# Performance work log

Hardware: AMD Instinct MI355X
Metric: run time of the kernel (lower is better)

The kernel has to match this reference:

```python
import jax, jax.numpy as jnp
import numpy as np

B, NZ, L = 8, 16, 512
E, DM, NH, HD = 256, 512, 16, 32
FF, NL, E1D, PDIM, PMAX = 1024, 8, 32, 64, 24
EPS_LN = 1e-5
EPS_D = 1e-12


def _ln(x, g, b):
    m = jnp.mean(x, axis=-1, keepdims=True)
    v = jnp.mean((x - m) ** 2, axis=-1, keepdims=True)
    return (x - m) / jnp.sqrt(v + EPS_LN) * g + b


def setup_inputs() -> dict:
    key = jax.random.key(0)
    ks = iter(jax.random.split(key, 32))
    rn = lambda shape, fan: jax.random.normal(next(ks), shape, jnp.float32) / np.float32(np.sqrt(fan))
    inp = {
        "z": jax.random.normal(next(ks), (B, NZ, L), jnp.float32),
        "x": jax.random.uniform(next(ks), (B, 20, L), jnp.float32),
        # embeddings
        "pos_table": rn((2 * PMAX + 1, PDIM), 1.0),
        "aa_table": rn((20, E1D), 1.0),
        # embed_x: Linear(nz,E), relu, Linear(E,E)
        "ex_w1": rn((NZ, E), NZ), "ex_b1": jnp.zeros((E,), jnp.float32),
        "ex_w2": rn((E, E), E), "ex_b2": jnp.zeros((E,), jnp.float32),
        # per-layer stacked params
        "Wq": rn((NL, E, DM), E), "Wk": rn((NL, E, DM), E), "Wv": rn((NL, E, DM), E),
        "Wo": rn((NL, DM, E), DM), "bo": jnp.zeros((NL, E), jnp.float32),
        "W2d": rn((NL, PDIM, NH), PDIM), "b2d": jnp.zeros((NL, NH), jnp.float32),
        "W1": rn((NL, E + E1D, FF), E + E1D), "b1": jnp.zeros((NL, FF), jnp.float32),
        "W2": rn((NL, FF, E), FF), "b2": jnp.zeros((NL, E), jnp.float32),
        "g1": jnp.ones((NL, E), jnp.float32), "be1": jnp.zeros((NL, E), jnp.float32),
        "g2": jnp.ones((NL, E), jnp.float32), "be2": jnp.zeros((NL, E), jnp.float32),
        # mlp_3d: Linear(E,E), relu, Linear(E,3)
        "m3_w1": rn((E, E), E), "m3_b1": jnp.zeros((E,), jnp.float32),
        "m3_w2": rn((E, 3), E), "m3_b2": jnp.zeros((3,), jnp.float32),
    }
    return inp


def reference(z, x, pos_table, aa_table, ex_w1, ex_b1, ex_w2, ex_b2,
              Wq, Wk, Wv, Wo, bo, W2d, b2d, W1, b1, W2, b2,
              g1, be1, g2, be2, m3_w1, m3_b1, m3_w2, m3_b2):
    Bn, _, Ln = z.shape
    h = jnp.transpose(z, (0, 2, 1))  # (B, L, nz)
    # relative-position bins: argmin over integer bins == clip to [-PMAX, PMAX]
    rel = jnp.arange(Ln)[None, :] - jnp.arange(Ln)[:, None]
    bins = jnp.clip(rel, -PMAX, PMAX) + PMAX
    pe = pos_table[bins]  # (L, L, PDIM), batch-replicated
    e_aa = aa_table[jnp.argmax(x, axis=1)]  # (B, L, E1D)
    # embed_x MLP
    h = jax.nn.relu(h @ ex_w1 + ex_b1) @ ex_w2 + ex_b2  # (B, L, E)
    scale = np.float32(1.0 / np.sqrt(DM))  # dp_attn_norm='d_model'
    for i in range(NL):
        q = (h @ Wq[i]).reshape(Bn, Ln, NH, HD) * scale
        k = (h @ Wk[i]).reshape(Bn, Ln, NH, HD)
        v = (h @ Wv[i]).reshape(Bn, Ln, NH, HD)
        # learned pairwise bias: mlp_2d then transpose(1,3).transpose(2,3) -> bias[h,i,j] = out[i,j,h]
        bias = jnp.einsum('lmp,ph->hlm', pe, W2d[i]) + b2d[i][:, None, None]
        scores = jnp.einsum('blhd,bmhd->bhlm', q, k) + bias[None]
        attn = jax.nn.softmax(scores, axis=-1)
        o = jnp.einsum('bhlm,bmhd->blhd', attn, v).reshape(Bn, Ln, DM)
        h = _ln(h + (o @ Wo[i] + bo[i]), g1[i], be1[i])
        um = jnp.concatenate([h, e_aa], axis=-1)  # (B, L, E+E1D)
        s2 = jax.nn.relu(um @ W1[i] + b1[i]) @ W2[i] + b2[i]
        h = _ln(h + s2, g2[i], be2[i])
    r = jax.nn.relu(h @ m3_w1 + m3_b1) @ m3_w2 + m3_b2  # (B, L, 3)
    # distance map (get_coords=False path)
    d = jnp.sqrt(jnp.sum((r[:, None, :, :] - r[:, :, None, :]) ** 2, axis=-1) + EPS_D)
    return d  # (B, L, L)
```

## Files before the change

kernel.cpp:

```cpp
#include <hip/hip_runtime.h>
#include <math.h>

constexpr int Bn = 8, NZ = 16, Ln = 512;
constexpr int E = 256, DM = 512, NH = 16, HD = 32;
constexpr int FF = 1024, NL = 8, E1D = 32, PDIM = 64, PMAX = 24;
constexpr int ROWS = Bn * Ln;
constexpr float QSCALE = 0.04419417382415922f;

typedef __attribute__((ext_vector_type(8))) short bf16x8;
typedef __attribute__((ext_vector_type(4))) float floatx4;

__device__ inline unsigned short f2b(float f) {
  union { float f; unsigned u; } v; v.f = f;
  unsigned r = (v.u + 0x7FFF + ((v.u >> 16) & 1)) >> 16;
  return (unsigned short)r;
}
__device__ inline float b2f(unsigned short u) {
  union { unsigned u; float f; } v; v.u = ((unsigned)u) << 16; return v.f;
}

__global__ __launch_bounds__(256) void transpose_qkv(
    const float* __restrict__ Wq, const float* __restrict__ Wk,
    const float* __restrict__ Wv, unsigned short* __restrict__ qkvT)
{
  __shared__ float t[32][33];
  int zb = blockIdx.z;
  int which = zb / NL, l = zb % NL;
  const float* s = (which == 0 ? Wq : which == 1 ? Wk : Wv) + (size_t)l * E * DM;
  unsigned short* d = qkvT + (size_t)l * 3 * DM * E + (size_t)which * DM * E;
  int c0 = blockIdx.x * 32, r0 = blockIdx.y * 32;
  int tx = threadIdx.x & 31, ty = threadIdx.x >> 5;
  #pragma unroll
  for (int i = 0; i < 4; ++i)
    t[ty + i * 8][tx] = s[(size_t)(r0 + ty + i * 8) * DM + c0 + tx];
  __syncthreads();
  #pragma unroll
  for (int i = 0; i < 4; ++i)
    d[(size_t)(c0 + ty + i * 8) * E + r0 + tx] = f2b(t[tx][ty + i * 8]);
}

__global__ __launch_bounds__(256) void transpose_bf16(
    const float* __restrict__ src, unsigned short* __restrict__ dst,
    int R, int C, size_t sls, size_t dls)
{
  __shared__ float t[32][33];
  int l = blockIdx.z;
  int c0 = blockIdx.x * 32, r0 = blockIdx.y * 32;
  int tx = threadIdx.x & 31, ty = threadIdx.x >> 5;
  const float* s = src + (size_t)l * sls;
  unsigned short* d = dst + (size_t)l * dls;
  #pragma unroll
  for (int i = 0; i < 4; ++i)
    t[ty + i * 8][tx] = s[(size_t)(r0 + ty + i * 8) * C + c0 + tx];
  __syncthreads();
  #pragma unroll
  for (int i = 0; i < 4; ++i)
    d[(size_t)(c0 + ty + i * 8) * R + r0 + tx] = f2b(t[tx][ty + i * 8]);
}

__global__ __launch_bounds__(256) void embed1_kernel(
    const float* __restrict__ z, const float* __restrict__ x,
    const float* __restrict__ aa,
    const float* __restrict__ w1, const float* __restrict__ b1,
    float* __restrict__ t0, unsigned short* __restrict__ umb)
{
  int row = blockIdx.x;
  int b = row >> 9, l = row & (Ln - 1);
  int t = threadIdx.x;
  __shared__ float zs[NZ];
  __shared__ int am_s;
  if (t < NZ) zs[t] = z[((size_t)b * NZ + t) * Ln + l];
  if (t == 0) {
    const float* xp = x + (size_t)b * 20 * Ln + l;
    int am = 0; float bv = xp[0];
    for (int c = 1; c < 20; ++c) { float vv = xp[(size_t)c * Ln]; if (vv > bv) { bv = vv; am = c; } }
    am_s = am;
  }
  __syncthreads();
  float a1 = b1[t];
  #pragma unroll
  for (int nz = 0; nz < NZ; ++nz) a1 += zs[nz] * w1[nz * E + t];
  t0[(size_t)row * E + t] = fmaxf(a1, 0.f);
  if (t < E1D) umb[(size_t)row * (E + E1D) + E + t] = f2b(aa[am_s * E1D + t]);
}

__global__ __launch_bounds__(256) void bias_kernel(
    const float* __restrict__ pos, const float* __restrict__ W2d,
    const float* __restrict__ b2d, float* __restrict__ bias49)
{
  int layer = blockIdx.x;
  for (int idx = threadIdx.x; idx < NH * 49; idx += 256) {
    int hh = idx / 49, bin = idx % 49;
    float acc = b2d[layer * NH + hh];
    for (int p = 0; p < PDIM; ++p)
      acc += pos[bin * PDIM + p] * W2d[((size_t)layer * PDIM + p) * NH + hh];
    bias49[(size_t)layer * NH * 49 + hh * 49 + bin] = acc;
  }
}

template<int BM, int BN, bool BIAS, bool RELU, bool OUTBF16, bool QKV>
__global__ __launch_bounds__(256) void gemm_mfma(
    const unsigned short* __restrict__ A, const unsigned short* __restrict__ Bt,
    const float* __restrict__ bias,
    float* __restrict__ Cf, unsigned short* __restrict__ Cb, int N, int K)
{
  constexpr int MT = BM / 32, NT = BN / 32;
  __shared__ __align__(16) unsigned short As[BM][40];
  __shared__ __align__(16) unsigned short Bs[BN][40];
  const int tid = threadIdx.x;
  const int wave = tid >> 6, ln = tid & 63;
  const int quad = ln >> 4, l16 = ln & 15;
  const int wm = wave >> 1, wn = wave & 1;
  const int m0 = blockIdx.y * BM, n0 = blockIdx.x * BN;

  floatx4 acc[MT][NT] = {};

  for (int kb = 0; kb < K; kb += 32) {
    __syncthreads();
    #pragma unroll
    for (int it = 0; it < BM / 64; ++it) {
      int c = tid + it * 256;
      int row = c >> 2, cc = (c & 3) * 8;
      *(float4*)&As[row][cc] = *(const float4*)(A + (size_t)(m0 + row) * K + kb + cc);
    }
    #pragma unroll
    for (int it = 0; it < BN / 64; ++it) {
      int c = tid + it * 256;
      int row = c >> 2, cc = (c & 3) * 8;
      *(float4*)&Bs[row][cc] = *(const float4*)(Bt + (size_t)(n0 + row) * K + kb + cc);
    }
    __syncthreads();
    bf16x8 af[MT], bfr[NT];
    #pragma unroll
    for (int i = 0; i < MT; ++i)
      af[i] = *(const bf16x8*)&As[wm * (BM / 2) + i * 16 + l16][quad * 8];
    #pragma unroll
    for (int j = 0; j < NT; ++j)
      bfr[j] = *(const bf16x8*)&Bs[wn * (BN / 2) + j * 16 + l16][quad * 8];
    #pragma unroll
    for (int i = 0; i < MT; ++i)
      #pragma unroll
      for (int j = 0; j < NT; ++j)
        acc[i][j] = __builtin_amdgcn_mfma_f32_16x16x32_bf16(af[i], bfr[j], acc[i][j], 0, 0, 0);
  }

  #pragma unroll
  for (int i = 0; i < MT; ++i)
    #pragma unroll
    for (int j = 0; j < NT; ++j) {
      int col = n0 + wn * (BN / 2) + j * 16 + l16;
      float bv = BIAS ? bias[col] : 0.f;
      float sc = QKV ? (col < 512 ? QSCALE : 1.f) : 1.f;
      #pragma unroll
      for (int r = 0; r < 4; ++r) {
        int rowg = m0 + wm * (BM / 2) + i * 16 + quad * 4 + r;
        float v = acc[i][j][r] * sc + bv;
        if (RELU) v = fmaxf(v, 0.f);
        if (OUTBF16) Cb[(size_t)rowg * N + col] = f2b(v);
        else Cf[(size_t)rowg * N + col] = v;
      }
    }
}

__global__ __launch_bounds__(256) void gemm_n256(
    const unsigned short* __restrict__ A, const unsigned short* __restrict__ Bt,
    const float* __restrict__ bias, const float* __restrict__ resid,
    float* __restrict__ Cf, int K)
{
  __shared__ __align__(16) unsigned short As[32][72];
  __shared__ __align__(16) unsigned short Bs[32][72];
  const int tid = threadIdx.x;
  const int wave = tid >> 6, ln = tid & 63;
  const int quad = ln >> 4, l16 = ln & 15;
  const int wm = wave >> 1, wn = wave & 1;
  const int m0 = blockIdx.y * 32, n0 = blockIdx.x * 32;
  const int srow = tid >> 3, scol = (tid & 7) * 8;

  floatx4 acc = {};

  for (int kb = 0; kb < K; kb += 64) {
    float4 ta = *(const float4*)(A + (size_t)(m0 + srow) * K + kb + scol);
    float4 tb = *(const float4*)(Bt + (size_t)(n0 + srow) * K + kb + scol);
    __syncthreads();
    *(float4*)&As[srow][scol] = ta;
    *(float4*)&Bs[srow][scol] = tb;
    __syncthreads();
    #pragma unroll
    for (int kc = 0; kc < 2; ++kc) {
      bf16x8 af = *(const bf16x8*)&As[wm * 16 + l16][kc * 32 + quad * 8];
      bf16x8 bf = *(const bf16x8*)&Bs[wn * 16 + l16][kc * 32 + quad * 8];
      acc = __builtin_amdgcn_mfma_f32_16x16x32_bf16(af, bf, acc, 0, 0, 0);
    }
  }

  const int col = n0 + wn * 16 + l16;
  const float bv = bias[col];
  #pragma unroll
  for (int r = 0; r < 4; ++r) {
    int rowg = m0 + wm * 16 + quad * 4 + r;
    Cf[(size_t)rowg * 256 + col] = acc[r] + bv + resid[(size_t)rowg * 256 + col];
  }
}

__global__ __launch_bounds__(256) void attn_kernel(
    const unsigned short* __restrict__ qkv, const float* __restrict__ bias49,
    unsigned short* __restrict__ o)
{
  const int i0 = blockIdx.x * 64;
  const int bh = blockIdx.y;
  const int b = bh >> 4, hh = bh & 15;
  const int tid = threadIdx.x;
  const int wave = tid >> 6, ln = tid & 63;
  const int quad = ln >> 4, l16 = ln & 15;

  __shared__ __align__(16) unsigned short Kt[64][40];
  __shared__ __align__(16) unsigned short Vt[32][72];
  __shared__ __align__(16) unsigned short Pw[4][2][16][72];
  __shared__ float bsh[49];

  if (tid < 49) bsh[tid] = bias49[hh * 49 + tid];

  const unsigned short* qkvb = qkv + (size_t)b * Ln * 1536;

  const int qrow = i0 + wave * 16 + l16;
  const bf16x8 qf = *(const bf16x8*)(qkvb + (size_t)qrow * 1536 + hh * 32 + quad * 8);

  float m[4], l[4];
  #pragma unroll
  for (int r = 0; r < 4; ++r) { m[r] = -1e30f; l[r] = 0.f; }
  floatx4 acc_o[2] = {};

  const int krow = tid >> 2, kch = (tid & 3) * 8;
  const int vkey = tid & 63, vch = (tid >> 6) * 8;

  for (int jt = 0; jt < 8; ++jt) {
    const int j0 = jt * 64;
    __syncthreads();
    *(float4*)&Kt[krow][kch] =
        *(const float4*)(qkvb + (size_t)(j0 + krow) * 1536 + 512 + hh * 32 + kch);
    bf16x8 vv = *(const bf16x8*)(qkvb + (size_t)(j0 + vkey) * 1536 + 1024 + hh * 32 + vch);
    #pragma unroll
    for (int i = 0; i < 8; ++i) Vt[vch + i][vkey] = (unsigned short)vv[i];
    __syncthreads();

    floatx4 s4[4];
    #pragma unroll
    for (int t = 0; t < 4; ++t) {
      bf16x8 kf = *(const bf16x8*)&Kt[16 * t + l16][quad * 8];
      s4[t] = __builtin_amdgcn_mfma_f32_16x16x32_bf16(qf, kf, (floatx4){0.f, 0.f, 0.f, 0.f}, 0, 0, 0);
    }
    const int relmin = j0 - (i0 + 63), relmax = j0 + 63 - i0;
    if (relmin >= PMAX) {
      float bc = bsh[48];
      #pragma unroll
      for (int t = 0; t < 4; ++t)
        #pragma unroll
        for (int r = 0; r < 4; ++r) s4[t][r] += bc;
    } else if (relmax <= -PMAX) {
      float bc = bsh[0];
      #pragma unroll
      for (int t = 0; t < 4; ++t)
        #pragma unroll
        for (int r = 0; r < 4; ++r) s4[t][r] += bc;
    } else {
      const int base_rel = (j0 + l16) - (i0 + wave * 16 + quad * 4);
      #pragma unroll
      for (int t = 0; t < 4; ++t)
        #pragma unroll
        for (int r = 0; r < 4; ++r) {
          int rel = base_rel + 16 * t - r;
          rel = rel < -PMAX ? -PMAX : (rel > PMAX ? PMAX : rel);
          s4[t][r] += bsh[rel + PMAX];
        }
    }

    float mloc[4], alpha[4], psum[4];
    #pragma unroll
    for (int r = 0; r < 4; ++r) {
      mloc[r] = fmaxf(fmaxf(s4[0][r], s4[1][r]), fmaxf(s4[2][r], s4[3][r]));
      #pragma unroll
      for (int off = 1; off < 16; off <<= 1)
        mloc[r] = fmaxf(mloc[r], __shfl_xor(mloc[r], off, 64));
      float mnew = fmaxf(m[r], mloc[r]);
      alpha[r] = __expf(m[r] - mnew);
      m[r] = mnew;
      psum[r] = 0.f;
    }
    #pragma unroll
    for (int t = 0; t < 4; ++t)
      #pragma unroll
      for (int r = 0; r < 4; ++r) {
        float p = __expf(s4[t][r] - m[r]);
        s4[t][r] = p;
        psum[r] += p;
      }
    #pragma unroll
    for (int r = 0; r < 4; ++r) {
      #pragma unroll
      for (int off = 1; off < 16; off <<= 1)
        psum[r] += __shfl_xor(psum[r], off, 64);
      l[r] = l[r] * alpha[r] + psum[r];
      acc_o[0][r] *= alpha[r];
      acc_o[1][r] *= alpha[r];
    }

    #pragma unroll
    for (int t = 0; t < 4; ++t)
      #pragma unroll
      for (int r = 0; r < 4; ++r) {
        float p = s4[t][r];
        unsigned short hi = f2b(p);
        unsigned short lo = f2b(p - b2f(hi));
        Pw[wave][0][quad * 4 + r][16 * t + l16] = hi;
        Pw[wave][1][quad * 4 + r][16 * t + l16] = lo;
      }

    #pragma unroll
    for (int kh = 0; kh < 2; ++kh) {
      bf16x8 phi = *(const bf16x8*)&Pw[wave][0][l16][kh * 32 + quad * 8];
      bf16x8 plo = *(const bf16x8*)&Pw[wave][1][l16][kh * 32 + quad * 8];
      #pragma unroll
      for (int nt = 0; nt < 2; ++nt) {
        bf16x8 vf = *(const bf16x8*)&Vt[nt * 16 + l16][kh * 32 + quad * 8];
        acc_o[nt] = __builtin_amdgcn_mfma_f32_16x16x32_bf16(phi, vf, acc_o[nt], 0, 0, 0);
        acc_o[nt] = __builtin_amdgcn_mfma_f32_16x16x32_bf16(plo, vf, acc_o[nt], 0, 0, 0);
      }
    }
  }

  #pragma unroll
  for (int r = 0; r < 4; ++r) {
    float inv = 1.f / l[r];
    size_t rowg = (size_t)b * Ln + i0 + wave * 16 + quad * 4 + r;
    #pragma unroll
    for (int nt = 0; nt < 2; ++nt)
      o[rowg * 512 + hh * 32 + nt * 16 + l16] = f2b(acc_o[nt][r] * inv);
  }
}

__global__ __launch_bounds__(256) void ln_kernel(
    const float* __restrict__ xin, const float* __restrict__ g,
    const float* __restrict__ be, float* __restrict__ hout,
    unsigned short* __restrict__ bout, int bstride)
{
  const int w = threadIdx.x >> 6, lane = threadIdx.x & 63;
  const size_t row = (size_t)blockIdx.x * 4 + w;
  const int c0 = lane * 4;
  float4 v = *(const float4*)(xin + row * E + c0);
  float s = v.x + v.y + v.z + v.w;
  float s2 = v.x * v.x + v.y * v.y + v.z * v.z + v.w * v.w;
  #pragma unroll
  for (int off = 1; off < 64; off <<= 1) {
    s += __shfl_xor(s, off, 64);
    s2 += __shfl_xor(s2, off, 64);
  }
  const float mean = s * (1.f / E);
  const float rstd = rsqrtf(s2 * (1.f / E) - mean * mean + 1e-5f);
  const float4 gv = *(const float4*)(g + c0);
  const float4 bv = *(const float4*)(be + c0);
  float4 y;
  y.x = (v.x - mean) * rstd * gv.x + bv.x;
  y.y = (v.y - mean) * rstd * gv.y + bv.y;
  y.z = (v.z - mean) * rstd * gv.z + bv.z;
  y.w = (v.w - mean) * rstd * gv.w + bv.w;
  *(float4*)(hout + row * E + c0) = y;
  ushort4 yb;
  yb.x = f2b(y.x); yb.y = f2b(y.y); yb.z = f2b(y.z); yb.w = f2b(y.w);
  *(ushort4*)(bout + row * (size_t)bstride + c0) = yb;
}

template<bool RELU, bool BIAS, bool MIRROR>
__global__ __launch_bounds__(256) void gemm64f(
    const float* __restrict__ A, const float* __restrict__ B,
    const float* __restrict__ bias, float* __restrict__ C,
    unsigned short* __restrict__ mir, int N, int K)
{
  __shared__ __align__(16) float As[16][64];
  __shared__ __align__(16) float Bss[16][68];
  const int tid = threadIdx.x;
  const int tx = tid & 15, ty = tid >> 4;
  const int m0 = blockIdx.y * 64, n0 = blockIdx.x * 64;
  const int arow = tid >> 2, acol = (tid & 3) * 4;
  const int brow = tid >> 6, bcol = tid & 63;
  float acc[4][4] = {};
  for (int kb = 0; kb < K; kb += 16) {
    __syncthreads();
    float4 av = *(const float4*)(A + (size_t)(m0 + arow) * K + kb + acol);
    As[acol + 0][arow] = av.x; As[acol + 1][arow] = av.y;
    As[acol + 2][arow] = av.z; As[acol + 3][arow] = av.w;
    #pragma unroll
    for (int kk = 0; kk < 4; ++kk)
      Bss[brow + kk * 4][bcol] = B[(size_t)(kb + brow + kk * 4) * N + n0 + bcol];
    __syncthreads();
    #pragma unroll
    for (int k = 0; k < 16; ++k) {
      float4 a = *(const float4*)&As[k][4 * ty];
      float4 b = *(const float4*)&Bss[k][4 * tx];
      float av4[4] = {a.x, a.y, a.z, a.w};
      float bv4[4] = {b.x, b.y, b.z, b.w};
      #pragma unroll
      for (int ii = 0; ii < 4; ++ii)
        #pragma unroll
        for (int jj = 0; jj < 4; ++jj)
          acc[ii][jj] += av4[ii] * bv4[jj];
    }
  }
  #pragma unroll
  for (int ii = 0; ii < 4; ++ii) {
    size_t row = (size_t)m0 + 4 * ty + ii;
    int col = n0 + 4 * tx;
    float4 vv;
    vv.x = acc[ii][0]; vv.y = acc[ii][1]; vv.z = acc[ii][2]; vv.w = acc[ii][3];
    if (BIAS) {
      float4 bb = *(const float4*)(bias + col);
      vv.x += bb.x; vv.y += bb.y; vv.z += bb.z; vv.w += bb.w;
    }
    if (RELU) {
      vv.x = fmaxf(vv.x, 0.f); vv.y = fmaxf(vv.y, 0.f);
      vv.z = fmaxf(vv.z, 0.f); vv.w = fmaxf(vv.w, 0.f);
    }
    *(float4*)(C + row * N + col) = vv;
    if (MIRROR) {
      ushort4 mv;
      mv.x = f2b(vv.x); mv.y = f2b(vv.y); mv.z = f2b(vv.z); mv.w = f2b(vv.w);
      *(ushort4*)(mir + row * N + col) = mv;
    }
  }
}

__global__ __launch_bounds__(256) void final_r_kernel(
    const float* __restrict__ t1, const float* __restrict__ w2,
    const float* __restrict__ b2, float* __restrict__ r)
{
  int row = blockIdx.x, t = threadIdx.x;
  float xv = t1[(size_t)row * E + t];
  float p0 = xv * w2[t * 3 + 0];
  float p1 = xv * w2[t * 3 + 1];
  float p2 = xv * w2[t * 3 + 2];
  #pragma unroll
  for (int off = 32; off > 0; off >>= 1) {
    p0 += __shfl_down(p0, off, 64);
    p1 += __shfl_down(p1, off, 64);
    p2 += __shfl_down(p2, off, 64);
  }
  __shared__ float red[4][3];
  if ((t & 63) == 0) { int w = t >> 6; red[w][0] = p0; red[w][1] = p1; red[w][2] = p2; }
  __syncthreads();
  if (t < 3)
    r[(size_t)row * 3 + t] = red[0][t] + red[1][t] + red[2][t] + red[3][t] + b2[t];
}

__global__ __launch_bounds__(512) void dist_kernel(
    const float* __restrict__ r, float* __restrict__ out)
{
  int bi = blockIdx.x;
  int j = threadIdx.x;
  int b = bi >> 9;
  float x0 = r[(size_t)bi * 3 + 0];
  float y0 = r[(size_t)bi * 3 + 1];
  float z0 = r[(size_t)bi * 3 + 2];
  const float* rj = r + ((size_t)b * Ln + j) * 3;
  float dx = rj[0] - x0, dy = rj[1] - y0, dz = rj[2] - z0;
  out[(size_t)bi * Ln + j] = sqrtf(dx * dx + dy * dy + dz * dz + 1e-12f);
}

extern "C" void kernel_launch(void* const* d_in, const int* in_sizes, int n_in,
                              void* d_out, int out_size, void* d_ws, size_t ws_size,
                              hipStream_t stream)
{
  const float* z     = (const float*)d_in[0];
  const float* x     = (const float*)d_in[1];
  const float* pos   = (const float*)d_in[2];
  const float* aa    = (const float*)d_in[3];
  const float* ex_w1 = (const float*)d_in[4];
  const float* ex_b1 = (const float*)d_in[5];
  const float* ex_w2 = (const float*)d_in[6];
  const float* ex_b2 = (const float*)d_in[7];
  const float* Wq    = (const float*)d_in[8];
  const float* Wk    = (const float*)d_in[9];
  const float* Wv    = (const float*)d_in[10];
  const float* Wo    = (const float*)d_in[11];
  const float* bo    = (const float*)d_in[12];
  const float* W2d   = (const float*)d_in[13];
  const float* b2d   = (const float*)d_in[14];
  const float* W1    = (const float*)d_in[15];
  const float* b1    = (const float*)d_in[16];
  const float* W2    = (const float*)d_in[17];
  const float* b2    = (const float*)d_in[18];
  const float* g1    = (const float*)d_in[19];
  const float* be1   = (const float*)d_in[20];
  const float* g2    = (const float*)d_in[21];
  const float* be2   = (const float*)d_in[22];
  const float* m3w1  = (const float*)d_in[23];
  const float* m3b1  = (const float*)d_in[24];
  const float* m3w2  = (const float*)d_in[25];
  const float* m3b2  = (const float*)d_in[26];

  float* ws     = (float*)d_ws;
  float* h      = ws;
  float* t0     = h + (size_t)ROWS * E;
  float* r      = t0 + (size_t)ROWS * E;
  float* bias49 = r + (size_t)ROWS * 3;
  unsigned short* us = (unsigned short*)(bias49 + NL * NH * 49);
  unsigned short* hb   = us;
  unsigned short* umb  = hb  + (size_t)ROWS * E;
  unsigned short* qkvb = umb + (size_t)ROWS * (E + E1D);
  unsigned short* ob   = qkvb + (size_t)ROWS * 3 * DM;
  unsigned short* t1b  = ob  + (size_t)ROWS * DM;
  unsigned short* qkvT = t1b + (size_t)ROWS * FF;
  unsigned short* WoT  = qkvT + (size_t)NL * 3 * DM * E;
  unsigned short* W1T  = WoT  + (size_t)NL * E * DM;
  unsigned short* W2T  = W1T  + (size_t)NL * FF * (E+E1D);
  float* tmp = t0;
  float* t1f = (float*)t1b;

  transpose_qkv<<<dim3(DM/32, E/32, 3*NL), 256, 0, stream>>>(Wq, Wk, Wv, qkvT);
  transpose_bf16<<<dim3(E/32, DM/32, NL), 256, 0, stream>>>(
      Wo, WoT, DM, E, (size_t)DM * E, (size_t)DM * E);
  transpose_bf16<<<dim3(FF/32, (E+E1D)/32, NL), 256, 0, stream>>>(
      W1, W1T, E + E1D, FF, (size_t)(E+E1D) * FF, (size_t)(E+E1D) * FF);
  transpose_bf16<<<dim3(E/32, FF/32, NL), 256, 0, stream>>>(
      W2, W2T, FF, E, (size_t)FF * E, (size_t)FF * E);

  embed1_kernel<<<ROWS, 256, 0, stream>>>(z, x, aa, ex_w1, ex_b1, t0, umb);
  gemm64f<false,true,true><<<dim3(E/64, ROWS/64), 256, 0, stream>>>(
      t0, ex_w2, ex_b2, h, hb, E, E);
  bias_kernel<<<NL, 256, 0, stream>>>(pos, W2d, b2d, bias49);

  for (int i = 0; i < NL; ++i) {
    gemm_mfma<64,128,false,false,true,true><<<dim3(12, 64), 256, 0, stream>>>(
        hb, qkvT + (size_t)i * 3 * DM * E, nullptr, nullptr, qkvb, 3 * DM, E);
    attn_kernel<<<dim3(Ln/64, Bn*NH), 256, 0, stream>>>(
        qkvb, bias49 + (size_t)i * NH * 49, ob);
    gemm_n256<<<dim3(E/32, ROWS/32), 256, 0, stream>>>(
        ob, WoT + (size_t)i * DM * E, bo + (size_t)i * E, h, tmp, DM);
    ln_kernel<<<ROWS/4, 256, 0, stream>>>(tmp, g1 + (size_t)i * E, be1 + (size_t)i * E, h, umb, E + E1D);
    gemm_mfma<64,64,true,true,true,false><<<dim3(FF/64, ROWS/64), 256, 0, stream>>>(
        umb, W1T + (size_t)i * FF * (E+E1D), b1 + (size_t)i * FF, nullptr, t1b, FF, E + E1D);
    gemm_n256<<<dim3(E/32, ROWS/32), 256, 0, stream>>>(
        t1b, W2T + (size_t)i * E * FF, b2 + (size_t)i * E, h, tmp, FF);
    ln_kernel<<<ROWS/4, 256, 0, stream>>>(tmp, g2 + (size_t)i * E, be2 + (size_t)i * E, h, hb, E);
  }

  gemm64f<true,true,false><<<dim3(E/64, ROWS/64), 256, 0, stream>>>(
      h, m3w1, m3b1, t1f, nullptr, E, E);
  final_r_kernel<<<ROWS, 256, 0, stream>>>(t1f, m3w2, m3b2, r);
  dist_kernel<<<ROWS, 512, 0, stream>>>(r, (float*)d_out);
}
```

Baseline: 858.0 us.

## Double-buffer shared-memory tiles with register prefetch in GEMM and attention kernels

Converts the MFMA GEMMs, the N=256 residual GEMM, the attention K/V tile loads and the fp32 GEMM to double-buffered shared memory. The next K-tile is prefetched into registers while the current tile is being computed, which leaves one barrier per iteration instead of two. The goal is to hide global-load latency behind MFMA/FMA work. The cost is twice the LDS footprint and more live registers, which may lower occupancy.

```diff
diff --git a/kernel.cpp b/kernel.cpp
--- a/kernel.cpp
+++ b/kernel.cpp
@@ -105,8 +105,9 @@
     float* __restrict__ Cf, unsigned short* __restrict__ Cb, int N, int K)
 {
   constexpr int MT = BM / 32, NT = BN / 32;
-  __shared__ __align__(16) unsigned short As[BM][40];
-  __shared__ __align__(16) unsigned short Bs[BN][40];
+  constexpr int AIT = BM / 64, BIT = BN / 64;
+  __shared__ __align__(16) unsigned short As[2][BM][40];
+  __shared__ __align__(16) unsigned short Bs[2][BN][40];
   const int tid = threadIdx.x;
   const int wave = tid >> 6, ln = tid & 63;
   const int quad = ln >> 4, l16 = ln & 15;
@@ -114,29 +115,53 @@
   const int m0 = blockIdx.y * BM, n0 = blockIdx.x * BN;
 
   floatx4 acc[MT][NT] = {};
-
-  for (int kb = 0; kb < K; kb += 32) {
-    __syncthreads();
-    #pragma unroll
-    for (int it = 0; it < BM / 64; ++it) {
-      int c = tid + it * 256;
-      int row = c >> 2, cc = (c & 3) * 8;
-      *(float4*)&As[row][cc] = *(const float4*)(A + (size_t)(m0 + row) * K + kb + cc);
-    }
-    #pragma unroll
-    for (int it = 0; it < BN / 64; ++it) {
-      int c = tid + it * 256;
-      int row = c >> 2, cc = (c & 3) * 8;
-      *(float4*)&Bs[row][cc] = *(const float4*)(Bt + (size_t)(n0 + row) * K + kb + cc);
+  float4 ra[AIT], rb[BIT];
+
+  #pragma unroll
+  for (int it = 0; it < AIT; ++it) {
+    int c = tid + it * 256; int row = c >> 2, cc = (c & 3) * 8;
+    ra[it] = *(const float4*)(A + (size_t)(m0 + row) * K + cc);
+  }
+  #pragma unroll
+  for (int it = 0; it < BIT; ++it) {
+    int c = tid + it * 256; int row = c >> 2, cc = (c & 3) * 8;
+    rb[it] = *(const float4*)(Bt + (size_t)(n0 + row) * K + cc);
+  }
+
+  const int nk = K >> 5;
+  for (int t = 0; t < nk; ++t) {
+    const int cur = t & 1;
+    #pragma unroll
+    for (int it = 0; it < AIT; ++it) {
+      int c = tid + it * 256; int row = c >> 2, cc = (c & 3) * 8;
+      *(float4*)&As[cur][row][cc] = ra[it];
+    }
+    #pragma unroll
+    for (int it = 0; it < BIT; ++it) {
+      int c = tid + it * 256; int row = c >> 2, cc = (c & 3) * 8;
+      *(float4*)&Bs[cur][row][cc] = rb[it];
+    }
+    if (t + 1 < nk) {
+      const int kb = (t + 1) * 32;
+      #pragma unroll
+      for (int it = 0; it < AIT; ++it) {
+        int c = tid + it * 256; int row = c >> 2, cc = (c & 3) * 8;
+        ra[it] = *(const float4*)(A + (size_t)(m0 + row) * K + kb + cc);
+      }
+      #pragma unroll
+      for (int it = 0; it < BIT; ++it) {
+        int c = tid + it * 256; int row = c >> 2, cc = (c & 3) * 8;
+        rb[it] = *(const float4*)(Bt + (size_t)(n0 + row) * K + kb + cc);
+      }
     }
     __syncthreads();
     bf16x8 af[MT], bfr[NT];
     #pragma unroll
     for (int i = 0; i < MT; ++i)
-      af[i] = *(const bf16x8*)&As[wm * (BM / 2) + i * 16 + l16][quad * 8];
+      af[i] = *(const bf16x8*)&As[cur][wm * (BM / 2) + i * 16 + l16][quad * 8];
     #pragma unroll
     for (int j = 0; j < NT; ++j)
-      bfr[j] = *(const bf16x8*)&Bs[wn * (BN / 2) + j * 16 + l16][quad * 8];
+      bfr[j] = *(const bf16x8*)&Bs[cur][wn * (BN / 2) + j * 16 + l16][quad * 8];
     #pragma unroll
     for (int i = 0; i < MT; ++i)
       #pragma unroll
@@ -167,8 +192,8 @@
     const float* __restrict__ bias, const float* __restrict__ resid,
     float* __restrict__ Cf, int K)
 {
-  __shared__ __align__(16) unsigned short As[32][72];
-  __shared__ __align__(16) unsigned short Bs[32][72];
+  __shared__ __align__(16) unsigned short As[2][32][72];
+  __shared__ __align__(16) unsigned short Bs[2][32][72];
   const int tid = threadIdx.x;
   const int wave = tid >> 6, ln = tid & 63;
   const int quad = ln >> 4, l16 = ln & 15;
@@ -176,19 +201,27 @@
   const int m0 = blockIdx.y * 32, n0 = blockIdx.x * 32;
   const int srow = tid >> 3, scol = (tid & 7) * 8;
 
+  const unsigned short* ap = A + (size_t)(m0 + srow) * K + scol;
+  const unsigned short* bp = Bt + (size_t)(n0 + srow) * K + scol;
+
   floatx4 acc = {};
-
-  for (int kb = 0; kb < K; kb += 64) {
-    float4 ta = *(const float4*)(A + (size_t)(m0 + srow) * K + kb + scol);
-    float4 tb = *(const float4*)(Bt + (size_t)(n0 + srow) * K + kb + scol);
+  float4 ta = *(const float4*)ap;
+  float4 tb = *(const float4*)bp;
+
+  const int nk = K >> 6;
+  for (int t = 0; t < nk; ++t) {
+    const int cur = t & 1;
+    *(float4*)&As[cur][srow][scol] = ta;
+    *(float4*)&Bs[cur][srow][scol] = tb;
+    if (t + 1 < nk) {
+      ta = *(const float4*)(ap + (size_t)(t + 1) * 64);
+      tb = *(const float4*)(bp + (size_t)(t + 1) * 64);
+    }
     __syncthreads();
-    *(float4*)&As[srow][scol] = ta;
-    *(float4*)&Bs[srow][scol] = tb;
-    __syncthreads();
     #pragma unroll
     for (int kc = 0; kc < 2; ++kc) {
-      bf16x8 af = *(const bf16x8*)&As[wm * 16 + l16][kc * 32 + quad * 8];
-      bf16x8 bf = *(const bf16x8*)&Bs[wn * 16 + l16][kc * 32 + quad * 8];
+      bf16x8 af = *(const bf16x8*)&As[cur][wm * 16 + l16][kc * 32 + quad * 8];
+      bf16x8 bf = *(const bf16x8*)&Bs[cur][wn * 16 + l16][kc * 32 + quad * 8];
       acc = __builtin_amdgcn_mfma_f32_16x16x32_bf16(af, bf, acc, 0, 0, 0);
     }
   }
@@ -213,8 +246,8 @@
   const int wave = tid >> 6, ln = tid & 63;
   const int quad = ln >> 4, l16 = ln & 15;
 
-  __shared__ __align__(16) unsigned short Kt[64][40];
-  __shared__ __align__(16) unsigned short Vt[32][72];
+  __shared__ __align__(16) unsigned short Kt[2][64][40];
+  __shared__ __align__(16) unsigned short Vt[2][32][72];
   __shared__ __align__(16) unsigned short Pw[4][2][16][72];
   __shared__ float bsh[49];
 
@@ -232,21 +265,28 @@
 
   const int krow = tid >> 2, kch = (tid & 3) * 8;
   const int vkey = tid & 63, vch = (tid >> 6) * 8;
+  const unsigned short* kp = qkvb + (size_t)krow * 1536 + 512 + hh * 32 + kch;
+  const unsigned short* vp = qkvb + (size_t)vkey * 1536 + 1024 + hh * 32 + vch;
+
+  float4 kreg = *(const float4*)kp;
+  bf16x8 vreg = *(const bf16x8*)vp;
 
   for (int jt = 0; jt < 8; ++jt) {
     const int j0 = jt * 64;
+    const int cur = jt & 1;
+    *(float4*)&Kt[cur][krow][kch] = kreg;
+    #pragma unroll
+    for (int i = 0; i < 8; ++i) Vt[cur][vch + i][vkey] = (unsigned short)vreg[i];
+    if (jt < 7) {
+      kreg = *(const float4*)(kp + (size_t)(j0 + 64) * 1536);
+      vreg = *(const bf16x8*)(vp + (size_t)(j0 + 64) * 1536);
+    }
     __syncthreads();
-    *(float4*)&Kt[krow][kch] =
-        *(const float4*)(qkvb + (size_t)(j0 + krow) * 1536 + 512 + hh * 32 + kch);
-    bf16x8 vv = *(const bf16x8*)(qkvb + (size_t)(j0 + vkey) * 1536 + 1024 + hh * 32 + vch);
-    #pragma unroll
-    for (int i = 0; i < 8; ++i) Vt[vch + i][vkey] = (unsigned short)vv[i];
-    __syncthreads();
 
     floatx4 s4[4];
     #pragma unroll
     for (int t = 0; t < 4; ++t) {
-      bf16x8 kf = *(const bf16x8*)&Kt[16 * t + l16][quad * 8];
+      bf16x8 kf = *(const bf16x8*)&Kt[cur][16 * t + l16][quad * 8];
       s4[t] = __builtin_amdgcn_mfma_f32_16x16x32_bf16(qf, kf, (floatx4){0.f, 0.f, 0.f, 0.f}, 0, 0, 0);
     }
     const int relmin = j0 - (i0 + 63), relmax = j0 + 63 - i0;
@@ -321,7 +361,7 @@
       bf16x8 plo = *(const bf16x8*)&Pw[wave][1][l16][kh * 32 + quad * 8];
       #pragma unroll
       for (int nt = 0; nt < 2; ++nt) {
-        bf16x8 vf = *(const bf16x8*)&Vt[nt * 16 + l16][kh * 32 + quad * 8];
+        bf16x8 vf = *(const bf16x8*)&Vt[cur][nt * 16 + l16][kh * 32 + quad * 8];
         acc_o[nt] = __builtin_amdgcn_mfma_f32_16x16x32_bf16(phi, vf, acc_o[nt], 0, 0, 0);
         acc_o[nt] = __builtin_amdgcn_mfma_f32_16x16x32_bf16(plo, vf, acc_o[nt], 0, 0, 0);
       }
@@ -375,27 +415,41 @@
     const float* __restrict__ bias, float* __restrict__ C,
     unsigned short* __restrict__ mir, int N, int K)
 {
-  __shared__ __align__(16) float As[16][64];
-  __shared__ __align__(16) float Bss[16][68];
+  __shared__ __align__(16) float As[2][16][64];
+  __shared__ __align__(16) float Bss[2][16][68];
   const int tid = threadIdx.x;
   const int tx = tid & 15, ty = tid >> 4;
   const int m0 = blockIdx.y * 64, n0 = blockIdx.x * 64;
   const int arow = tid >> 2, acol = (tid & 3) * 4;
   const int brow = tid >> 6, bcol = tid & 63;
   float acc[4][4] = {};
-  for (int kb = 0; kb < K; kb += 16) {
+
+  float4 av = *(const float4*)(A + (size_t)(m0 + arow) * K + acol);
+  float bbr[4];
+  #pragma unroll
+  for (int kk = 0; kk < 4; ++kk)
+    bbr[kk] = B[(size_t)(brow + kk * 4) * N + n0 + bcol];
+
+  const int nk = K >> 4;
+  for (int t = 0; t < nk; ++t) {
+    const int cur = t & 1;
+    As[cur][acol + 0][arow] = av.x; As[cur][acol + 1][arow] = av.y;
+    As[cur][acol + 2][arow] = av.z; As[cur][acol + 3][arow] = av.w;
+    #pragma unroll
+    for (int kk = 0; kk < 4; ++kk)
+      Bss[cur][brow + kk * 4][bcol] = bbr[kk];
+    if (t + 1 < nk) {
+      const int kb = (t + 1) * 16;
+      av = *(const float4*)(A + (size_t)(m0 + arow) * K + kb + acol);
+      #pragma unroll
+      for (int kk = 0; kk < 4; ++kk)
+        bbr[kk] = B[(size_t)(kb + brow + kk * 4) * N + n0 + bcol];
+    }
     __syncthreads();
-    float4 av = *(const float4*)(A + (size_t)(m0 + arow) * K + kb + acol);
-    As[acol + 0][arow] = av.x; As[acol + 1][arow] = av.y;
-    As[acol + 2][arow] = av.z; As[acol + 3][arow] = av.w;
-    #pragma unroll
-    for (int kk = 0; kk < 4; ++kk)
-      Bss[brow + kk * 4][bcol] = B[(size_t)(kb + brow + kk * 4) * N + n0 + bcol];
-    __syncthreads();
     #pragma unroll
     for (int k = 0; k < 16; ++k) {
-      float4 a = *(const float4*)&As[k][4 * ty];
-      float4 b = *(const float4*)&Bss[k][4 * tx];
+      float4 a = *(const float4*)&As[cur][k][4 * ty];
+      float4 b = *(const float4*)&Bss[cur][k][4 * tx];
       float av4[4] = {a.x, a.y, a.z, a.w};
       float bv4[4] = {b.x, b.y, b.z, b.w};
       #pragma unroll
```

After: 918.4 us. 1.07x slower.

## Use direct global-to-LDS loads with XOR-swizzled shared tiles in GEMMs

Applied to the files above, without the earlier changes.

Both MFMA GEMM kernels now stage A and B tiles with global_load_lds (direct global-to-LDS DMA of 16 bytes per lane) instead of loading through registers and writing to shared memory. The padded LDS rows are replaced by unpadded rows with an XOR swizzle on the 8-element chunk index to avoid bank conflicts, and the fragment reads apply the matching swizzle. This cuts register traffic and VALU/LDS-store instructions in the load path. It relies on the intrinsic's wave-uniform LDS base layout and removes the prefetch-into-register overlap the n256 kernel previously had.

```diff
diff --git a/kernel.cpp b/kernel.cpp
--- a/kernel.cpp
+++ b/kernel.cpp
@@ -17,6 +17,12 @@
 }
 __device__ inline float b2f(unsigned short u) {
   union { unsigned u; float f; } v; v.u = ((unsigned)u) << 16; return v.f;
+}
+
+__device__ inline void gll16(const void* g, void* l) {
+  __builtin_amdgcn_global_load_lds(
+      (const __attribute__((address_space(1))) void*)g,
+      (__attribute__((address_space(3))) void*)l, 16, 0, 0);
 }
 
 __global__ __launch_bounds__(256) void transpose_qkv(
@@ -105,38 +111,38 @@
     float* __restrict__ Cf, unsigned short* __restrict__ Cb, int N, int K)
 {
   constexpr int MT = BM / 32, NT = BN / 32;
-  __shared__ __align__(16) unsigned short As[BM][40];
-  __shared__ __align__(16) unsigned short Bs[BN][40];
+  __shared__ __align__(16) unsigned short As[BM][32];
+  __shared__ __align__(16) unsigned short Bs[BN][32];
   const int tid = threadIdx.x;
   const int wave = tid >> 6, ln = tid & 63;
   const int quad = ln >> 4, l16 = ln & 15;
   const int wm = wave >> 1, wn = wave & 1;
   const int m0 = blockIdx.y * BM, n0 = blockIdx.x * BN;
 
+  const int lrow = ln >> 2, chunk = ln & 3;
+  const int schunk = chunk ^ ((lrow >> 1) & 3);
+  const unsigned short* aSrc = A + (size_t)(m0 + wave * 16 + lrow) * K + schunk * 8;
+  const unsigned short* bSrc = Bt + (size_t)(n0 + wave * 16 + lrow) * K + schunk * 8;
+  const int rkey = (l16 >> 1) & 3;
+
   floatx4 acc[MT][NT] = {};
 
   for (int kb = 0; kb < K; kb += 32) {
     __syncthreads();
     #pragma unroll
-    for (int it = 0; it < BM / 64; ++it) {
-      int c = tid + it * 256;
-      int row = c >> 2, cc = (c & 3) * 8;
-      *(float4*)&As[row][cc] = *(const float4*)(A + (size_t)(m0 + row) * K + kb + cc);
-    }
-    #pragma unroll
-    for (int it = 0; it < BN / 64; ++it) {
-      int c = tid + it * 256;
-      int row = c >> 2, cc = (c & 3) * 8;
-      *(float4*)&Bs[row][cc] = *(const float4*)(Bt + (size_t)(n0 + row) * K + kb + cc);
-    }
+    for (int it = 0; it < BM / 64; ++it)
+      gll16(aSrc + (size_t)it * 64 * K + kb, &As[it * 64 + wave * 16][0]);
+    #pragma unroll
+    for (int it = 0; it < BN / 64; ++it)
+      gll16(bSrc + (size_t)it * 64 * K + kb, &Bs[it * 64 + wave * 16][0]);
     __syncthreads();
     bf16x8 af[MT], bfr[NT];
     #pragma unroll
     for (int i = 0; i < MT; ++i)
-      af[i] = *(const bf16x8*)&As[wm * (BM / 2) + i * 16 + l16][quad * 8];
+      af[i] = *(const bf16x8*)&As[wm * (BM / 2) + i * 16 + l16][(quad ^ rkey) * 8];
     #pragma unroll
     for (int j = 0; j < NT; ++j)
-      bfr[j] = *(const bf16x8*)&Bs[wn * (BN / 2) + j * 16 + l16][quad * 8];
+      bfr[j] = *(const bf16x8*)&Bs[wn * (BN / 2) + j * 16 + l16][(quad ^ rkey) * 8];
     #pragma unroll
     for (int i = 0; i < MT; ++i)
       #pragma unroll
@@ -167,28 +173,31 @@
     const float* __restrict__ bias, const float* __restrict__ resid,
     float* __restrict__ Cf, int K)
 {
-  __shared__ __align__(16) unsigned short As[32][72];
-  __shared__ __align__(16) unsigned short Bs[32][72];
+  __shared__ __align__(16) unsigned short As[32][64];
+  __shared__ __align__(16) unsigned short Bs[32][64];
   const int tid = threadIdx.x;
   const int wave = tid >> 6, ln = tid & 63;
   const int quad = ln >> 4, l16 = ln & 15;
   const int wm = wave >> 1, wn = wave & 1;
   const int m0 = blockIdx.y * 32, n0 = blockIdx.x * 32;
-  const int srow = tid >> 3, scol = (tid & 7) * 8;
+
+  const int lrow = ln >> 3, chunk = ln & 7;
+  const int schunk = chunk ^ lrow;
+  const unsigned short* ap = A + (size_t)(m0 + wave * 8 + lrow) * K + schunk * 8;
+  const unsigned short* bp = Bt + (size_t)(n0 + wave * 8 + lrow) * K + schunk * 8;
+  const int rkey = l16 & 7;
 
   floatx4 acc = {};
 
   for (int kb = 0; kb < K; kb += 64) {
-    float4 ta = *(const float4*)(A + (size_t)(m0 + srow) * K + kb + scol);
-    float4 tb = *(const float4*)(Bt + (size_t)(n0 + srow) * K + kb + scol);
-    __syncthreads();
-    *(float4*)&As[srow][scol] = ta;
-    *(float4*)&Bs[srow][scol] = tb;
+    __syncthreads();
+    gll16(ap + kb, &As[wave * 8][0]);
+    gll16(bp + kb, &Bs[wave * 8][0]);
     __syncthreads();
     #pragma unroll
     for (int kc = 0; kc < 2; ++kc) {
-      bf16x8 af = *(const bf16x8*)&As[wm * 16 + l16][kc * 32 + quad * 8];
-      bf16x8 bf = *(const bf16x8*)&Bs[wn * 16 + l16][kc * 32 + quad * 8];
+      bf16x8 af = *(const bf16x8*)&As[wm * 16 + l16][((kc * 4 + quad) ^ rkey) * 8];
+      bf16x8 bf = *(const bf16x8*)&Bs[wn * 16 + l16][((kc * 4 + quad) ^ rkey) * 8];
       acc = __builtin_amdgcn_mfma_f32_16x16x32_bf16(af, bf, acc, 0, 0, 0);
     }
   }
```

New measurement: 841.9 us. Within noise of the previous version (-1.9%).
